# Performance work log

Measured on AMD Instinct MI355X. Metric: run time of the kernel, lower is better.

Reference implementation:

```python
import jax, jax.numpy as jnp
import numpy as np

N, IN_DIM, OUT_DIM = 8192, 512, 512
ALPHA = 0.2  # leaky relu negative slope
NEG_BIG = -9e15

def _xavier(key, shape, gain=1.414):
    fan_in, fan_out = shape[0], shape[1]
    bound = gain * np.sqrt(6.0 / (fan_in + fan_out))
    return jax.random.uniform(key, shape, jnp.float32, -bound, bound)

def setup_inputs() -> dict:
    key = jax.random.key(0)
    k1, k2, k3, k4 = jax.random.split(key, 4)
    h = jax.random.normal(k1, (N, IN_DIM), jnp.float32)
    adj = jax.random.randint(k2, (N, N), 0, 2, jnp.int32)
    W = _xavier(k3, (IN_DIM, OUT_DIM))
    a = _xavier(k4, (2 * OUT_DIM, 1))
    return {"h": h, "adj": adj, "W": W, "a": a}

def reference(h, adj, W, a):
    Wh = h @ W                              # [N, out]
    # e_ij = leakyrelu(a1 . Wh_i + a2 . Wh_j) without the O(N^2*2d) concat
    a1 = a[:OUT_DIM, 0]                     # [out]
    a2 = a[OUT_DIM:, 0]                     # [out]
    f1 = Wh @ a1                            # [N]
    f2 = Wh @ a2                            # [N]
    e = jax.nn.leaky_relu(f1[:, None] + f2[None, :], negative_slope=ALPHA)
    e = jnp.where(adj > 0, e, NEG_BIG)
    attention = jax.nn.softmax(e, axis=1)   # dropout is identity in eval mode
    h_prime = attention @ Wh                # [N, out]
    return jax.nn.elu(h_prime)              # concat=True branch
```

## Files before the change

kernel.cpp:

```cpp
#include <hip/hip_runtime.h>
#include <stdint.h>

#define NN   8192
#define DIN  512
#define DOUT 512
#define ALPHA 0.2f

typedef float          floatx4  __attribute__((ext_vector_type(4)));
typedef float          floatx2  __attribute__((ext_vector_type(2)));
typedef short          shortx8  __attribute__((ext_vector_type(8)));
typedef unsigned short ushortx4 __attribute__((ext_vector_type(4)));
typedef int            intx4    __attribute__((ext_vector_type(4)));

__device__ inline unsigned short f2bf(float x) {
    union { float f; unsigned u; } v; v.f = x;
    return (unsigned short)((v.u + 0x7FFFu + ((v.u >> 16) & 1u)) >> 16);
}
__device__ inline unsigned encf(float x) {
    union { float f; unsigned u; } v; v.f = x;
    return (v.u & 0x80000000u) ? ~v.u : (v.u | 0x80000000u);
}
__device__ inline float decf(unsigned e) {
    union { float f; unsigned u; } v;
    v.u = (e & 0x80000000u) ? (e & 0x7FFFFFFFu) : ~e;
    return v.f;
}
__device__ inline float lrelu(float x) { return fmaxf(x, ALPHA * x); }

__global__ __launch_bounds__(256) void pack_adj(const int* __restrict__ adj,
                                                unsigned* __restrict__ bits) {
    const int row = blockIdx.x;
    const int t = threadIdx.x;
    const int w = t >> 6, lane = t & 63;
    const int* rp = adj + (size_t)row * NN;
#pragma unroll 4
    for (int it = 0; it < 32; ++it) {
        const int col = it * 256 + w * 64 + lane;
        const int v = __builtin_nontemporal_load(rp + col);
        const unsigned long long m = __ballot(v > 0);
        if (lane == 0) {
            const int kt = it * 8 + w * 2;
            bits[(size_t)kt * NN + row] = (unsigned)m;
            bits[(size_t)(kt + 1) * NN + row] = (unsigned)(m >> 32);
        }
    }
}

__global__ __launch_bounds__(256) void transpose_w(const float* __restrict__ W,
                                                   unsigned short* __restrict__ WT) {
    __shared__ float tile[32][33];
    const int t = threadIdx.x;
    const int x = t & 31, y = t >> 5;
    const int tr = (blockIdx.x >> 4) * 32, tc = (blockIdx.x & 15) * 32;
#pragma unroll
    for (int i = 0; i < 4; i++) {
        int r = y + i * 8;
        tile[r][x] = W[(size_t)(tr + r) * DOUT + tc + x];
    }
    __syncthreads();
#pragma unroll
    for (int i = 0; i < 4; i++) {
        int r = y + i * 8;
        WT[(size_t)(tc + r) * DIN + tr + x] = f2bf(tile[x][r]);
    }
}

__global__ __launch_bounds__(256) void gemm_wh(
    const float* __restrict__ h, const unsigned short* __restrict__ WT,
    const float* __restrict__ a, unsigned short* __restrict__ WhTt,
    float* __restrict__ f1, float* __restrict__ f2, unsigned* __restrict__ Menc)
{
    __shared__ float f1s[4][16], f2s[4][16];
    const int t = threadIdx.x;
    const int w = t >> 6, lane = t & 63, l15 = lane & 15, q = lane >> 4;
    const int r0 = blockIdx.x * 16;
    const int wc0 = w * 128;

    floatx4 acc[8];
    const floatx4 z4 = {0.f, 0.f, 0.f, 0.f};
#pragma unroll
    for (int j = 0; j < 8; j++) acc[j] = z4;

    const float* hp = &h[(size_t)(r0 + l15) * DIN + q * 8];
    const unsigned short* bp = &WT[(size_t)(wc0 + l15) * DIN + q * 8];

    floatx4 hA[2][2];
    shortx8 bB[2][8];
    hA[0][0] = *(const floatx4*)hp;
    hA[0][1] = *(const floatx4*)(hp + 4);
#pragma unroll
    for (int nt = 0; nt < 8; nt++)
        bB[0][nt] = *(const shortx8*)(bp + (size_t)nt * 16 * DIN);

#pragma unroll 2
    for (int it = 0; it < 16; ++it) {
        const int c = it & 1, n = c ^ 1;
        const int kn = ((it + 1) & 15) * 32;
        hA[n][0] = *(const floatx4*)(hp + kn);
        hA[n][1] = *(const floatx4*)(hp + kn + 4);
#pragma unroll
        for (int nt = 0; nt < 8; nt++)
            bB[n][nt] = *(const shortx8*)(bp + (size_t)nt * 16 * DIN + kn);

        shortx8 af;
#pragma unroll
        for (int j = 0; j < 8; j++)
            af[j] = (short)f2bf(hA[c][j >> 2][j & 3]);
#pragma unroll
        for (int nt = 0; nt < 8; nt++)
            acc[nt] = __builtin_amdgcn_mfma_f32_16x16x32_bf16(af, bB[c][nt], acc[nt], 0, 0, 0);
    }

    float a1v[8], a2v[8];
#pragma unroll
    for (int nt = 0; nt < 8; nt++) {
        int col = wc0 + nt * 16 + l15;
        a1v[nt] = a[col];
        a2v[nt] = a[DOUT + col];
    }
    {
        const int kk0 = r0 + q * 4;
        const int tile_k = kk0 >> 5;
        const int qq = (kk0 >> 3) & 3;
        const int j0 = kk0 & 7;
#pragma unroll
        for (int nt = 0; nt < 8; nt++) {
            const int tile_n = w * 8 + nt;
            ushortx4 pk;
#pragma unroll
            for (int reg = 0; reg < 4; reg++) pk[reg] = f2bf(acc[nt][reg]);
            *(ushortx4*)&WhTt[(((size_t)tile_k * 32 + tile_n) << 9) + qq * 128 + l15 * 8 + j0] = pk;
        }
    }
    float s1a[4], s2a[4];
#pragma unroll
    for (int reg = 0; reg < 4; reg++) {
        float s1 = 0.f, s2 = 0.f;
#pragma unroll
        for (int nt = 0; nt < 8; nt++) {
            s1 += acc[nt][reg] * a1v[nt];
            s2 += acc[nt][reg] * a2v[nt];
        }
        s1 += __shfl_xor(s1, 1, 64); s2 += __shfl_xor(s2, 1, 64);
        s1 += __shfl_xor(s1, 2, 64); s2 += __shfl_xor(s2, 2, 64);
        s1 += __shfl_xor(s1, 4, 64); s2 += __shfl_xor(s2, 4, 64);
        s1 += __shfl_xor(s1, 8, 64); s2 += __shfl_xor(s2, 8, 64);
        s1a[reg] = s1; s2a[reg] = s2;
    }
    if (l15 == 0) {
#pragma unroll
        for (int reg = 0; reg < 4; reg++) {
            f1s[w][q * 4 + reg] = s1a[reg];
            f2s[w][q * 4 + reg] = s2a[reg];
        }
    }
    __syncthreads();
    if (t < 16) {
        float v1 = f1s[0][t] + f1s[1][t] + f1s[2][t] + f1s[3][t];
        float v2 = f2s[0][t] + f2s[1][t] + f2s[2][t] + f2s[3][t];
        f1[r0 + t] = v1;
        f2[r0 + t] = v2;
        float mx = v2;
        mx = fmaxf(mx, __shfl_xor(mx, 1, 64));
        mx = fmaxf(mx, __shfl_xor(mx, 2, 64));
        mx = fmaxf(mx, __shfl_xor(mx, 4, 64));
        mx = fmaxf(mx, __shfl_xor(mx, 8, 64));
        if (t == 0) atomicMax(Menc, encf(mx));
    }
}

__global__ __launch_bounds__(1024, 4) void gat_agg(
    const unsigned* __restrict__ bits, const unsigned short* __restrict__ WhTt,
    const float* __restrict__ f1, const float* __restrict__ f2,
    const unsigned* __restrict__ Menc, float* __restrict__ out)
{
    __shared__ __align__(16) unsigned short pbuf[2][2][32 * 40];
    __shared__ float red2[32][260];
    __shared__ float lsp[2][16][32];
    __shared__ float linv[32];

    const int t = threadIdx.x;
    const int w = t >> 6, lane = t & 63, l15 = lane & 15, q = lane >> 4;
    const int ks = w >> 3, cw = w & 7;
    const int u = cw * 64 + lane;
    const int prow = u & 31, pkc = u >> 5;
    const int r0 = blockIdx.x * 32;

    const float M = decf(*Menc);
    const float f1v = f1[r0 + prow];
    const float mi = lrelu(f1v + M);

    floatx4 acc[2][4];
    const floatx4 z4 = {0.f, 0.f, 0.f, 0.f};
#pragma unroll
    for (int i = 0; i < 2; i++)
#pragma unroll
        for (int j = 0; j < 4; j++) acc[i][j] = z4;
    float ls = 0.f;

    const unsigned short* bpp = WhTt + (((size_t)(ks * 128) * 32 + cw * 4) << 9) + lane * 8;
    const unsigned* mbp = bits + (size_t)(ks * 128) * NN + r0 + prow;
    const float* fpp = f2 + ks * 4096 + pkc * 2;

    unsigned mkr[2];
    floatx2  ffr[2];
    shortx8  breg[2][4];

    mkr[0] = mbp[0];
    mkr[1] = mbp[NN];
    ffr[0] = *(const floatx2*)fpp;
    ffr[1] = *(const floatx2*)(fpp + 32);
    {
        const unsigned mk = mkr[0];
        float e0 = lrelu(f1v + ffr[0][0]) - mi;
        float e1 = lrelu(f1v + ffr[0][1]) - mi;
        float p0 = __expf(e0), p1 = __expf(e1);
        p0 = (mk >> (pkc * 2)) & 1u ? p0 : 0.f;
        p1 = (mk >> (pkc * 2 + 1)) & 1u ? p1 : 0.f;
        ls += p0 + p1;
        unsigned d = __builtin_amdgcn_perm(__float_as_uint(p1), __float_as_uint(p0), 0x07060302u);
        *(unsigned*)&pbuf[ks][0][prow * 40 + pkc * 2] = d;
    }
#pragma unroll
    for (int nt = 0; nt < 4; nt++)
        breg[0][nt] = *(const shortx8*)(bpp + nt * 512);
    __syncthreads();

#pragma unroll 2
    for (int it = 0; it < 128; ++it) {
        const int c = it & 1, n = c ^ 1;
        const int nx = (it + 1) & 127;
        const int nx2 = (it + 2) & 127;

#pragma unroll
        for (int nt = 0; nt < 4; nt++)
            breg[n][nt] = *(const shortx8*)(bpp + (size_t)nx * 16384 + nt * 512);
        const unsigned mk_n = mkr[n];
        const floatx2 ff_n = ffr[n];
        mkr[c] = mbp[(size_t)nx2 * NN];
        ffr[c] = *(const floatx2*)(fpp + nx2 * 32);

        {
            float e0 = lrelu(f1v + ff_n[0]) - mi;
            float e1 = lrelu(f1v + ff_n[1]) - mi;
            float p0 = __expf(e0), p1 = __expf(e1);
            p0 = (mk_n >> (pkc * 2)) & 1u ? p0 : 0.f;
            p1 = (mk_n >> (pkc * 2 + 1)) & 1u ? p1 : 0.f;
            ls += p0 + p1;
            unsigned d = __builtin_amdgcn_perm(__float_as_uint(p1), __float_as_uint(p0), 0x07060302u);
            *(unsigned*)&pbuf[ks][n][prow * 40 + pkc * 2] = d;
        }

        const shortx8 af0 = *(const shortx8*)&pbuf[ks][c][l15 * 40 + q * 8];
        const shortx8 af1 = *(const shortx8*)&pbuf[ks][c][(16 + l15) * 40 + q * 8];
#pragma unroll
        for (int nt = 0; nt < 4; nt++) {
            acc[0][nt] = __builtin_amdgcn_mfma_f32_16x16x32_bf16(af0, breg[c][nt], acc[0][nt], 0, 0, 0);
            acc[1][nt] = __builtin_amdgcn_mfma_f32_16x16x32_bf16(af1, breg[c][nt], acc[1][nt], 0, 0, 0);
        }
        __syncthreads();
    }
    {
        const unsigned mk = mbp[0];
        const floatx2 ff = *(const floatx2*)fpp;
        float e0 = lrelu(f1v + ff[0]) - mi;
        float e1 = lrelu(f1v + ff[1]) - mi;
        float p0 = __expf(e0), p1 = __expf(e1);
        p0 = (mk >> (pkc * 2)) & 1u ? p0 : 0.f;
        p1 = (mk >> (pkc * 2 + 1)) & 1u ? p1 : 0.f;
        ls -= p0 + p1;
    }

    lsp[ks][pkc][prow] = ls;
    __syncthreads();
    if (t < 32) {
        float s = 0.f;
#pragma unroll
        for (int g = 0; g < 2; g++)
#pragma unroll
            for (int kc = 0; kc < 16; kc++) s += lsp[g][kc][t];
        linv[t] = 1.f / s;
    }
    __syncthreads();

#pragma unroll 1
    for (int half = 0; half < 2; ++half) {
        const int inHalf = (cw >> 2) == half;
        const int colb = (cw & 3) * 64;
        if (ks == 1 && inHalf) {
#pragma unroll
            for (int mt = 0; mt < 2; mt++)
#pragma unroll
                for (int nt = 0; nt < 4; nt++) {
                    const int col = colb + nt * 16 + l15;
#pragma unroll
                    for (int reg = 0; reg < 4; reg++)
                        red2[mt * 16 + q * 4 + reg][col] = acc[mt][nt][reg];
                }
        }
        __syncthreads();
        if (ks == 0 && inHalf) {
#pragma unroll
            for (int mt = 0; mt < 2; mt++)
#pragma unroll
                for (int nt = 0; nt < 4; nt++) {
                    const int col = colb + nt * 16 + l15;
#pragma unroll
                    for (int reg = 0; reg < 4; reg++) {
                        const int row = mt * 16 + q * 4 + reg;
                        float x = (acc[mt][nt][reg] + red2[row][col]) * linv[row];
                        x = (x > 0.f) ? x : (__expf(x) - 1.f);
                        out[(size_t)(r0 + row) * DOUT + half * 256 + col] = x;
                    }
                }
        }
        __syncthreads();
    }
}

extern "C" void kernel_launch(void* const* d_in, const int* in_sizes, int n_in,
                              void* d_out, int out_size, void* d_ws, size_t ws_size,
                              hipStream_t stream) {
    const float* h   = (const float*)d_in[0];
    const int*   adj = (const int*)d_in[1];
    const float* W   = (const float*)d_in[2];
    const float* a   = (const float*)d_in[3];
    float* out = (float*)d_out;

    char* ws = (char*)d_ws;
    unsigned short* WT    = (unsigned short*)ws;
    unsigned short* WhTt  = (unsigned short*)(ws + 524288);
    unsigned*       bits  = (unsigned*)(ws + 8912896);
    float*          f1    = (float*)(ws + 17301504);
    float*          f2    = (float*)(ws + 17334272);
    unsigned*       Menc  = (unsigned*)(ws + 17367040);

    hipMemsetAsync(Menc, 0, 4, stream);
    pack_adj<<<NN, 256, 0, stream>>>(adj, bits);
    transpose_w<<<256, 256, 0, stream>>>(W, WT);
    gemm_wh<<<512, 256, 0, stream>>>(h, WT, a, WhTt, f1, f2, Menc);
    gat_agg<<<256, 1024, 0, stream>>>(bits, WhTt, f1, f2, Menc, out);
}
```

Baseline: 531.3 us.

## Fuse adjacency masking into aggregation kernel and drop bit-packing pass

Removes the separate pack_adj kernel that converted the int32 adjacency matrix into a transposed bitmask. The aggregation kernel now streams adj rows directly with nontemporal 8-byte loads, prefetched two iterations ahead. The thread-to-(row, column-chunk) mapping is changed so each row's loads are contiguous. This saves one full kernel launch plus the bitmask write and re-read, but the main loop now pulls the 256 MB adjacency from HBM with a short prefetch distance, which may expose memory latency inside the MFMA loop. The last-iteration wraparound correction is replaced by an it<127 guard.

```diff
diff --git a/kernel.cpp b/kernel.cpp
--- a/kernel.cpp
+++ b/kernel.cpp
@@ -10,7 +10,7 @@
 typedef float          floatx2  __attribute__((ext_vector_type(2)));
 typedef short          shortx8  __attribute__((ext_vector_type(8)));
 typedef unsigned short ushortx4 __attribute__((ext_vector_type(4)));
-typedef int            intx4    __attribute__((ext_vector_type(4)));
+typedef int            intx2    __attribute__((ext_vector_type(2)));
 
 __device__ inline unsigned short f2bf(float x) {
     union { float f; unsigned u; } v; v.f = x;
@@ -26,25 +26,6 @@
     return v.f;
 }
 __device__ inline float lrelu(float x) { return fmaxf(x, ALPHA * x); }
-
-__global__ __launch_bounds__(256) void pack_adj(const int* __restrict__ adj,
-                                                unsigned* __restrict__ bits) {
-    const int row = blockIdx.x;
-    const int t = threadIdx.x;
-    const int w = t >> 6, lane = t & 63;
-    const int* rp = adj + (size_t)row * NN;
-#pragma unroll 4
-    for (int it = 0; it < 32; ++it) {
-        const int col = it * 256 + w * 64 + lane;
-        const int v = __builtin_nontemporal_load(rp + col);
-        const unsigned long long m = __ballot(v > 0);
-        if (lane == 0) {
-            const int kt = it * 8 + w * 2;
-            bits[(size_t)kt * NN + row] = (unsigned)m;
-            bits[(size_t)(kt + 1) * NN + row] = (unsigned)(m >> 32);
-        }
-    }
-}
 
 __global__ __launch_bounds__(256) void transpose_w(const float* __restrict__ W,
                                                    unsigned short* __restrict__ WT) {
@@ -170,7 +151,7 @@
 }
 
 __global__ __launch_bounds__(1024, 4) void gat_agg(
-    const unsigned* __restrict__ bits, const unsigned short* __restrict__ WhTt,
+    const int* __restrict__ adj, const unsigned short* __restrict__ WhTt,
     const float* __restrict__ f1, const float* __restrict__ f2,
     const unsigned* __restrict__ Menc, float* __restrict__ out)
 {
@@ -183,7 +164,7 @@
     const int w = t >> 6, lane = t & 63, l15 = lane & 15, q = lane >> 4;
     const int ks = w >> 3, cw = w & 7;
     const int u = cw * 64 + lane;
-    const int prow = u & 31, pkc = u >> 5;
+    const int prow = u >> 4, pkc = u & 15;
     const int r0 = blockIdx.x * 32;
 
     const float M = decf(*Menc);
@@ -199,24 +180,22 @@
     float ls = 0.f;
 
     const unsigned short* bpp = WhTt + (((size_t)(ks * 128) * 32 + cw * 4) << 9) + lane * 8;
-    const unsigned* mbp = bits + (size_t)(ks * 128) * NN + r0 + prow;
+    const int* arp = adj + (size_t)(r0 + prow) * NN + ks * 4096 + pkc * 2;
     const float* fpp = f2 + ks * 4096 + pkc * 2;
 
-    unsigned mkr[2];
+    intx2    adjr[2];
     floatx2  ffr[2];
     shortx8  breg[2][4];
 
-    mkr[0] = mbp[0];
-    mkr[1] = mbp[NN];
+    adjr[0] = __builtin_nontemporal_load((const intx2*)arp);
+    adjr[1] = __builtin_nontemporal_load((const intx2*)(arp + 32));
     ffr[0] = *(const floatx2*)fpp;
     ffr[1] = *(const floatx2*)(fpp + 32);
     {
-        const unsigned mk = mkr[0];
-        float e0 = lrelu(f1v + ffr[0][0]) - mi;
-        float e1 = lrelu(f1v + ffr[0][1]) - mi;
-        float p0 = __expf(e0), p1 = __expf(e1);
-        p0 = (mk >> (pkc * 2)) & 1u ? p0 : 0.f;
-        p1 = (mk >> (pkc * 2 + 1)) & 1u ? p1 : 0.f;
+        float p0 = __expf(lrelu(f1v + ffr[0][0]) - mi);
+        float p1 = __expf(lrelu(f1v + ffr[0][1]) - mi);
+        p0 = (adjr[0][0] > 0) ? p0 : 0.f;
+        p1 = (adjr[0][1] > 0) ? p1 : 0.f;
         ls += p0 + p1;
         unsigned d = __builtin_amdgcn_perm(__float_as_uint(p1), __float_as_uint(p0), 0x07060302u);
         *(unsigned*)&pbuf[ks][0][prow * 40 + pkc * 2] = d;
@@ -235,17 +214,16 @@
 #pragma unroll
         for (int nt = 0; nt < 4; nt++)
             breg[n][nt] = *(const shortx8*)(bpp + (size_t)nx * 16384 + nt * 512);
-        const unsigned mk_n = mkr[n];
+        const intx2   ad_n = adjr[n];
         const floatx2 ff_n = ffr[n];
-        mkr[c] = mbp[(size_t)nx2 * NN];
+        adjr[c] = __builtin_nontemporal_load((const intx2*)(arp + nx2 * 32));
         ffr[c] = *(const floatx2*)(fpp + nx2 * 32);
 
-        {
-            float e0 = lrelu(f1v + ff_n[0]) - mi;
-            float e1 = lrelu(f1v + ff_n[1]) - mi;
-            float p0 = __expf(e0), p1 = __expf(e1);
-            p0 = (mk_n >> (pkc * 2)) & 1u ? p0 : 0.f;
-            p1 = (mk_n >> (pkc * 2 + 1)) & 1u ? p1 : 0.f;
+        if (it < 127) {
+            float p0 = __expf(lrelu(f1v + ff_n[0]) - mi);
+            float p1 = __expf(lrelu(f1v + ff_n[1]) - mi);
+            p0 = (ad_n[0] > 0) ? p0 : 0.f;
+            p1 = (ad_n[1] > 0) ? p1 : 0.f;
             ls += p0 + p1;
             unsigned d = __builtin_amdgcn_perm(__float_as_uint(p1), __float_as_uint(p0), 0x07060302u);
             *(unsigned*)&pbuf[ks][n][prow * 40 + pkc * 2] = d;
@@ -259,16 +237,6 @@
             acc[1][nt] = __builtin_amdgcn_mfma_f32_16x16x32_bf16(af1, breg[c][nt], acc[1][nt], 0, 0, 0);
         }
         __syncthreads();
-    }
-    {
-        const unsigned mk = mbp[0];
-        const floatx2 ff = *(const floatx2*)fpp;
-        float e0 = lrelu(f1v + ff[0]) - mi;
-        float e1 = lrelu(f1v + ff[1]) - mi;
-        float p0 = __expf(e0), p1 = __expf(e1);
-        p0 = (mk >> (pkc * 2)) & 1u ? p0 : 0.f;
-        p1 = (mk >> (pkc * 2 + 1)) & 1u ? p1 : 0.f;
-        ls -= p0 + p1;
     }
 
     lsp[ks][pkc][prow] = ls;
@@ -330,14 +298,12 @@
     char* ws = (char*)d_ws;
     unsigned short* WT    = (unsigned short*)ws;
     unsigned short* WhTt  = (unsigned short*)(ws + 524288);
-    unsigned*       bits  = (unsigned*)(ws + 8912896);
-    float*          f1    = (float*)(ws + 17301504);
-    float*          f2    = (float*)(ws + 17334272);
-    unsigned*       Menc  = (unsigned*)(ws + 17367040);
+    float*          f1    = (float*)(ws + 8912896);
+    float*          f2    = (float*)(ws + 8945664);
+    unsigned*       Menc  = (unsigned*)(ws + 8978432);
 
     hipMemsetAsync(Menc, 0, 4, stream);
-    pack_adj<<<NN, 256, 0, stream>>>(adj, bits);
     transpose_w<<<256, 256, 0, stream>>>(W, WT);
     gemm_wh<<<512, 256, 0, stream>>>(h, WT, a, WhTt, f1, f2, Menc);
-    gat_agg<<<256, 1024, 0, stream>>>(bits, WhTt, f1, f2, Menc, out);
-}
+    gat_agg<<<256, 1024, 0, stream>>>(adj, WhTt, f1, f2, Menc, out);
+}
```

Result: faster. 501.4 us (-5.6%).
